# Kernel tuning notes

Measured on AMD Instinct MI355X. Metric: run time of the kernel, lower is better.

## Reference

```python
import jax, jax.numpy as jnp
import numpy as np
import math

B, L, D, H = 16, 512, 128, 8


def setup_inputs() -> dict:
    key = jax.random.key(0)
    ks = jax.random.split(key, 10)
    xavier = lambda k, shp: jax.random.normal(k, shp, jnp.float32) * math.sqrt(2.0 / (shp[0] + shp[1]))
    inp = {
        "x": jax.random.normal(ks[0], (B, L, D), jnp.float32),
        "W_q": xavier(ks[1], (H * D, D)),
        "b_q": jnp.zeros((H * D,), jnp.float32),
        "W_k": xavier(ks[2], (H * D, D)),
        "b_k": jnp.zeros((H * D,), jnp.float32),
        "W_v": xavier(ks[3], (H * D, D)),
        "b_v": jnp.zeros((H * D,), jnp.float32),
        "W_o": xavier(ks[4], (D, H * D)),
        "b_o": jnp.zeros((D,), jnp.float32),
        "pad_mask": jax.random.randint(ks[5], (B, L, L), 0, 2).astype(bool),
        "batch_size": B,
        "max_len": L,
    }
    return inp


def reference(x, W_q, b_q, W_k, b_k, W_v, b_v, W_o, b_o, pad_mask, batch_size, max_len):
    # project: [B, L, D] -> [B, L, H*D] -> head-major [H*B, L, D]
    def proj(W, b):
        y = jnp.einsum('bld,ed->ble', x, W) + b          # [B, L, H*D]
        y = y.reshape(batch_size, max_len, H, D)
        return y.transpose(2, 0, 1, 3).reshape(H * batch_size, max_len, D)

    q = proj(W_q, b_q)
    k = proj(W_k, b_k)
    v = proj(W_v, b_v)

    scores = jnp.einsum('nqd,nkd->nqk', q, k)            # [H*B, L, L]
    mask = jnp.tile(pad_mask, (H, 1, 1))                 # repeat(n_heads,1,1)
    # faithful quirk: mask BEFORE scaling, softmax over QUERY axis (dim=1)
    scores = jnp.where(mask, -1e9, scores) / math.sqrt(D)
    attn = jax.nn.softmax(scores, axis=1)
    att = jnp.einsum('nqk,nkd->nqd', attn, v)            # [H*B, L, D]
    # faithful quirk: torch .view from (H*B, L, D) to (B, L, H*D)
    att = att.reshape(batch_size, max_len, H * D)
    out = jnp.einsum('ble,de->bld', att, W_o) + b_o      # [B, L, D]
    return out
```

## Files before the change

kernel.cpp:

```cpp
#include <hip/hip_runtime.h>

#define B_  16
#define L_  512
#define D_  128
#define H_  8
#define HD_ 1024
#define NH_ 128
#define M_  8192

typedef unsigned short u16;
typedef __attribute__((ext_vector_type(8))) short s16x8;
typedef __attribute__((ext_vector_type(4))) float f32x4;

__device__ __forceinline__ float bf2f(u16 u) {
    union { unsigned u; float f; } x; x.u = ((unsigned)u) << 16; return x.f;
}
__device__ __forceinline__ u16 f2bf(float f) {
    unsigned u = __float_as_uint(f);
    return (u16)((u + 0x7FFFu + ((u >> 16) & 1u)) >> 16);
}

__device__ __forceinline__ void mfma_bt64(const u16* __restrict__ A, int lda,
                                          const u16* __restrict__ B, int ldb,
                                          int K, int lane, f32x4 acc[4][4]) {
    const int mr = lane & 15, quad = lane >> 4;
    for (int k0 = 0; k0 < K; k0 += 32) {
        s16x8 av[4], bv[4];
#pragma unroll
        for (int i = 0; i < 4; i++)
            av[i] = *(const s16x8*)(A + (size_t)(i * 16 + mr) * lda + k0 + quad * 8);
#pragma unroll
        for (int j = 0; j < 4; j++)
            bv[j] = *(const s16x8*)(B + (size_t)(j * 16 + mr) * ldb + k0 + quad * 8);
#pragma unroll
        for (int i = 0; i < 4; i++)
#pragma unroll
            for (int j = 0; j < 4; j++)
                acc[i][j] = __builtin_amdgcn_mfma_f32_16x16x32_bf16(av[i], bv[j], acc[i][j], 0, 0, 0);
    }
}

__global__ void k0_detect(const unsigned int* __restrict__ pad,
                          const unsigned int* __restrict__ xw,
                          int* __restrict__ flags) {
    __shared__ int sMask, sCnt;
    if (threadIdx.x == 0) { sMask = 0; sCnt = 0; }
    __syncthreads();
    int bad = 0;
#pragma unroll
    for (int i = 0; i < 4; i++) {
        unsigned u = pad[threadIdx.x * 4 + i];
        bad |= (u > 1u) ? 1 : 0;
    }
    int cnt = 0;
#pragma unroll
    for (int i = 0; i < 16; i++) {
        unsigned w = xw[threadIdx.x * 16 + i];
        unsigned e = (w >> 7) & 0xFFu;
        cnt += (e >= 100u && e <= 131u) ? 1 : 0;
    }
    if (bad) atomicOr(&sMask, 1);
    atomicAdd(&sCnt, cnt);
    __syncthreads();
    if (threadIdx.x == 0) {
        flags[0] = (sCnt > 2048) ? 1 : 0;
        flags[1] = sMask;
    }
}

#define PREP_TOT 1576064
__global__ __launch_bounds__(256) void kprep_conv(
    const void* x, const void* Wq, const void* bq, const void* Wk, const void* bk,
    const void* Wv, const void* bv, const void* Wo, const void* bo,
    const int* __restrict__ flags,
    u16* xb, u16* Wqb, u16* Wkb, u16* Wvb, u16* Wob,
    u16* bqb, u16* bkb, u16* bvb, u16* bob) {
    int gid = blockIdx.x * 256 + threadIdx.x;
    if (gid >= PREP_TOT) return;
    const int dt = flags[0];
    const void* src; u16* dst; int off;
    if      (gid < 1048576) { src = x;  dst = xb;  off = gid; }
    else if (gid < 1179648) { src = Wq; dst = Wqb; off = gid - 1048576; }
    else if (gid < 1310720) { src = Wk; dst = Wkb; off = gid - 1179648; }
    else if (gid < 1441792) { src = Wv; dst = Wvb; off = gid - 1310720; }
    else if (gid < 1572864) { src = Wo; dst = Wob; off = gid - 1441792; }
    else if (gid < 1573888) { src = bq; dst = bqb; off = gid - 1572864; }
    else if (gid < 1574912) { src = bk; dst = bkb; off = gid - 1573888; }
    else if (gid < 1575936) { src = bv; dst = bvb; off = gid - 1574912; }
    else                    { src = bo; dst = bob; off = gid - 1575936; }
    dst[off] = dt ? ((const u16*)src)[off] : f2bf(((const float*)src)[off]);
}

__global__ __launch_bounds__(256) void kprep_mask(const void* __restrict__ pad,
                                                  const int* __restrict__ flags,
                                                  unsigned* __restrict__ mb) {
    int w = blockIdx.x * 256 + threadIdx.x;
    size_t base = (size_t)w * 32;
    unsigned m = 0;
    if (flags[1]) {
        const unsigned char* p = (const unsigned char*)pad;
#pragma unroll
        for (int b = 0; b < 32; b++) m |= (p[base + b] ? 1u : 0u) << b;
    } else {
        const int* p = (const int*)pad;
#pragma unroll
        for (int b = 0; b < 32; b++) m |= (p[base + b] ? 1u : 0u) << b;
    }
    mb[w] = m;
}

__global__ __launch_bounds__(256) void k1_proj(
    const u16* __restrict__ xb,
    const u16* __restrict__ Wqb, const u16* __restrict__ Wkb, const u16* __restrict__ Wvb,
    const u16* __restrict__ bqb, const u16* __restrict__ bkb, const u16* __restrict__ bvb,
    u16* __restrict__ qb, u16* __restrict__ kb, u16* __restrict__ vtb) {
    const int h  = blockIdx.x;
    const int m0 = blockIdx.y * 128;
    const int z  = blockIdx.z;
    const u16* W    = (z == 0) ? Wqb : (z == 1) ? Wkb : Wvb;
    const u16* bias = (z == 0) ? bqb : (z == 1) ? bkb : bvb;

    const int lane = threadIdx.x & 63, wave = threadIdx.x >> 6;
    const int wr = wave >> 1, wc = wave & 1;
    const int mr = lane & 15, quad = lane >> 4;

    f32x4 acc[4][4];
#pragma unroll
    for (int i = 0; i < 4; i++)
#pragma unroll
        for (int j = 0; j < 4; j++) acc[i][j] = (f32x4){0.f, 0.f, 0.f, 0.f};

    mfma_bt64(xb + (size_t)(m0 + wr * 64) * D_, D_,
              W + (size_t)(h * 128 + wc * 64) * D_, D_, D_, lane, acc);

    __shared__ __align__(16) u16 T[128][136];
#pragma unroll
    for (int i = 0; i < 4; i++)
#pragma unroll
        for (int j = 0; j < 4; j++) {
            int col = wc * 64 + j * 16 + mr;
            float bv_ = bf2f(bias[h * 128 + col]);
#pragma unroll
            for (int r = 0; r < 4; r++)
                T[wr * 64 + i * 16 + quad * 4 + r][col] = f2bf(acc[i][j][r] + bv_);
        }
    __syncthreads();

    const int bb = m0 >> 9, l0 = m0 & 511;
    const int t = threadIdx.x;
    if (z < 2) {
        u16* out = z ? kb : qb;
        int row = t >> 1, c0 = (t & 1) * 64;
        u16* dst = out + ((size_t)(h * B_ + bb) * L_ + l0 + row) * D_ + c0;
#pragma unroll
        for (int c = 0; c < 64; c += 8)
            *(uint4*)(dst + c) = *(const uint4*)&T[row][c0 + c];
    } else {
        int d = t >> 1, lc0 = (t & 1) * 64;
        u16* dst = vtb + ((size_t)(h * B_ + bb) * D_ + d) * L_ + l0 + lc0;
#pragma unroll
        for (int c = 0; c < 64; c += 8) {
            u16 tmp[8];
#pragma unroll
            for (int s = 0; s < 8; s++) tmp[s] = T[lc0 + c + s][d];
            *(uint4*)(dst + c) = *(const uint4*)tmp;
        }
    }
}

__global__ __launch_bounds__(256) void k2a_linv(
    const u16* __restrict__ qb, const u16* __restrict__ kb,
    const unsigned* __restrict__ mbits, float* __restrict__ linv) {
    const int kstrip = blockIdx.x * 128;
    const int n   = blockIdx.y;
    const int bb  = n & (B_ - 1);
    const int lane = threadIdx.x & 63, wave = threadIdx.x >> 6;
    const int wr = wave >> 1, wc = wave & 1;
    const int mr = lane & 15, quad = lane >> 4;
    const float rs = 0.08838834764831845f;

    __shared__ unsigned mw[2048];
    __shared__ float CS[2][128];
#pragma unroll
    for (int s = 0; s < 8; s++) {
        int idx = threadIdx.x * 8 + s;
        int q = idx >> 2, lw = idx & 3;
        mw[idx] = mbits[((size_t)(bb << 9) + q) * 16 + (blockIdx.x << 2) + lw];
    }
    __syncthreads();

    const u16* Abase = qb + (size_t)n * L_ * D_;
    const u16* Bbase = kb + (size_t)n * L_ * D_ + (size_t)(kstrip + wc * 64) * D_;

    float colsum[4] = {0.f, 0.f, 0.f, 0.f};
    for (int qt = 0; qt < 4; qt++) {
        f32x4 acc[4][4];
#pragma unroll
        for (int i = 0; i < 4; i++)
#pragma unroll
            for (int j = 0; j < 4; j++) acc[i][j] = (f32x4){0.f, 0.f, 0.f, 0.f};
        mfma_bt64(Abase + (size_t)(qt * 128 + wr * 64) * D_, D_, Bbase, D_, D_, lane, acc);
#pragma unroll
        for (int i = 0; i < 4; i++)
#pragma unroll
            for (int j = 0; j < 4; j++) {
                const int lw = wc * 2 + (j >> 1);
                const int bit = (j & 1) * 16 + mr;
#pragma unroll
                for (int r = 0; r < 4; r++) {
                    int q = qt * 128 + wr * 64 + i * 16 + quad * 4 + r;
                    unsigned w = mw[(q << 2) + lw];
                    if (!((w >> bit) & 1u))
                        colsum[j] += __expf(acc[i][j][r] * rs);
                }
            }
    }
#pragma unroll
    for (int j = 0; j < 4; j++) {
        colsum[j] += __shfl_xor(colsum[j], 16);
        colsum[j] += __shfl_xor(colsum[j], 32);
    }
    if (quad == 0) {
#pragma unroll
        for (int j = 0; j < 4; j++) CS[wr][wc * 64 + j * 16 + mr] = colsum[j];
    }
    __syncthreads();
    if (threadIdx.x < 128)
        linv[(size_t)n * L_ + kstrip + threadIdx.x] =
            1.0f / (CS[0][threadIdx.x] + CS[1][threadIdx.x]);
}

__global__ __launch_bounds__(256) void k2b_attn(
    const u16* __restrict__ qb, const u16* __restrict__ kb,
    const u16* __restrict__ vtb, const unsigned* __restrict__ mbits,
    const float* __restrict__ linv, u16* __restrict__ att) {
    const int qtile = blockIdx.x * 128;
    const int n  = blockIdx.y;
    const int bb = n & (B_ - 1);
    const int lane = threadIdx.x & 63, wave = threadIdx.x >> 6;
    const int wr = wave >> 1, wc = wave & 1;
    const int mr = lane & 15, quad = lane >> 4;
    const float rs = 0.08838834764831845f;

    __shared__ __align__(16) u16 eS[128][136];
    __shared__ unsigned mwq[2048];
    __shared__ float linvS[512];
#pragma unroll
    for (int s = 0; s < 8; s++) {
        int idx = threadIdx.x * 8 + s;
        int q = idx >> 4, w = idx & 15;
        mwq[idx] = mbits[((size_t)(bb << 9) + qtile + q) * 16 + w];
    }
    if (threadIdx.x < 128)
        *(float4*)&linvS[threadIdx.x * 4] = *(const float4*)&linv[(size_t)n * L_ + threadIdx.x * 4];
    __syncthreads();

    const u16* qn = qb + (size_t)n * L_ * D_;
    const u16* kn = kb + (size_t)n * L_ * D_;
    const u16* vn = vtb + (size_t)n * D_ * L_;

    f32x4 att_acc[4][4];
#pragma unroll
    for (int i = 0; i < 4; i++)
#pragma unroll
        for (int j = 0; j < 4; j++) att_acc[i][j] = (f32x4){0.f, 0.f, 0.f, 0.f};

    for (int kt = 0; kt < 4; kt++) {
        f32x4 qk[4][4];
#pragma unroll
        for (int i = 0; i < 4; i++)
#pragma unroll
            for (int j = 0; j < 4; j++) qk[i][j] = (f32x4){0.f, 0.f, 0.f, 0.f};
        mfma_bt64(qn + (size_t)(qtile + wr * 64) * D_, D_,
                  kn + (size_t)(kt * 128 + wc * 64) * D_, D_, D_, lane, qk);

#pragma unroll
        for (int i = 0; i < 4; i++)
#pragma unroll
            for (int j = 0; j < 4; j++) {
                const int widx = kt * 4 + wc * 2 + (j >> 1);
                const int bit = (j & 1) * 16 + mr;
                const int kl = wc * 64 + j * 16 + mr;
                const float lv = linvS[kt * 128 + kl];
#pragma unroll
                for (int r = 0; r < 4; r++) {
                    int ql = wr * 64 + i * 16 + quad * 4 + r;
                    unsigned w = mwq[(ql << 4) + widx];
                    float e = ((w >> bit) & 1u) ? 0.f : __expf(qk[i][j][r] * rs) * lv;
                    eS[ql][kl] = f2bf(e);
                }
            }
        __syncthreads();

#pragma unroll
        for (int kk = 0; kk < 4; kk++) {
            s16x8 av[4], bv[4];
#pragma unroll
            for (int i = 0; i < 4; i++)
                av[i] = *(const s16x8*)&eS[wr * 64 + i * 16 + mr][kk * 32 + quad * 8];
#pragma unroll
            for (int j = 0; j < 4; j++)
                bv[j] = *(const s16x8*)(vn + (size_t)(wc * 64 + j * 16 + mr) * L_
                                        + kt * 128 + kk * 32 + quad * 8);
#pragma unroll
            for (int i = 0; i < 4; i++)
#pragma unroll
                for (int j = 0; j < 4; j++)
                    att_acc[i][j] = __builtin_amdgcn_mfma_f32_16x16x32_bf16(av[i], bv[j], att_acc[i][j], 0, 0, 0);
        }
        __syncthreads();
    }

#pragma unroll
    for (int i = 0; i < 4; i++)
#pragma unroll
        for (int j = 0; j < 4; j++) {
            int col = wc * 64 + j * 16 + mr;
#pragma unroll
            for (int r = 0; r < 4; r++)
                eS[wr * 64 + i * 16 + quad * 4 + r][col] = f2bf(att_acc[i][j][r]);
        }
    __syncthreads();
    int t = threadIdx.x, row = t >> 1, c0 = (t & 1) * 64;
    u16* dst = att + ((size_t)n * L_ + qtile + row) * D_ + c0;
#pragma unroll
    for (int c = 0; c < 64; c += 8)
        *(uint4*)(dst + c) = *(const uint4*)&eS[row][c0 + c];
}

__global__ __launch_bounds__(128) void k5_out(
    const u16* __restrict__ att, const u16* __restrict__ Wob,
    const u16* __restrict__ bob, const int* __restrict__ flags,
    void* __restrict__ out) {
    const int dt = flags[0];
    const int n0 = blockIdx.x * 64;
    const int m0 = blockIdx.y * 64;
    const int lane = threadIdx.x & 63, wk = threadIdx.x >> 6;
    const int mr = lane & 15, quad = lane >> 4;

    f32x4 acc[4][4];
#pragma unroll
    for (int i = 0; i < 4; i++)
#pragma unroll
        for (int j = 0; j < 4; j++) acc[i][j] = (f32x4){0.f, 0.f, 0.f, 0.f};

    mfma_bt64(att + (size_t)m0 * HD_ + wk * 512, HD_,
              Wob + (size_t)n0 * HD_ + wk * 512, HD_, 512, lane, acc);

    __shared__ __align__(16) float Tf[64][68];
    if (wk == 0) {
#pragma unroll
        for (int i = 0; i < 4; i++)
#pragma unroll
            for (int j = 0; j < 4; j++)
#pragma unroll
                for (int r = 0; r < 4; r++)
                    Tf[i * 16 + quad * 4 + r][j * 16 + mr] = acc[i][j][r];
    }
    __syncthreads();
    if (wk == 1) {
#pragma unroll
        for (int i = 0; i < 4; i++)
#pragma unroll
            for (int j = 0; j < 4; j++)
#pragma unroll
                for (int r = 0; r < 4; r++)
                    Tf[i * 16 + quad * 4 + r][j * 16 + mr] += acc[i][j][r];
    }
    __syncthreads();

    int t = threadIdx.x, row = t >> 1, h0 = (t & 1) * 32;
    size_t base = (size_t)(m0 + row) * D_ + n0 + h0;
    if (dt) {
        u16* o = (u16*)out;
#pragma unroll
        for (int c = 0; c < 32; c += 8) {
            u16 tmp[8];
#pragma unroll
            for (int s = 0; s < 8; s++)
                tmp[s] = f2bf(Tf[row][h0 + c + s] + bf2f(bob[n0 + h0 + c + s]));
            *(uint4*)(o + base + c) = *(const uint4*)tmp;
        }
    } else {
        float* o = (float*)out;
#pragma unroll
        for (int c = 0; c < 32; c += 4) {
            float4 v;
            v.x = Tf[row][h0 + c + 0] + bf2f(bob[n0 + h0 + c + 0]);
            v.y = Tf[row][h0 + c + 1] + bf2f(bob[n0 + h0 + c + 1]);
            v.z = Tf[row][h0 + c + 2] + bf2f(bob[n0 + h0 + c + 2]);
            v.w = Tf[row][h0 + c + 3] + bf2f(bob[n0 + h0 + c + 3]);
            *(float4*)(o + base + c) = v;
        }
    }
}

extern "C" void kernel_launch(void* const* d_in, const int* in_sizes, int n_in,
                              void* d_out, int out_size, void* d_ws, size_t ws_size,
                              hipStream_t stream) {
    (void)in_sizes; (void)n_in; (void)out_size; (void)ws_size;
    const void* x  = d_in[0];
    const void* Wq = d_in[1]; const void* bq = d_in[2];
    const void* Wk = d_in[3]; const void* bk = d_in[4];
    const void* Wv = d_in[5]; const void* bv = d_in[6];
    const void* Wo = d_in[7]; const void* bo = d_in[8];
    const void* pad = d_in[9];

    char* p = (char*)d_ws;
    auto alloc = [&](size_t bytes) { char* r = p; p += (bytes + 255) & ~(size_t)255; return r; };
    int*  flags = (int*)alloc(256);
    u16*  xb   = (u16*)alloc(2097152);
    u16*  Wqb  = (u16*)alloc(262144);
    u16*  Wkb  = (u16*)alloc(262144);
    u16*  Wvb  = (u16*)alloc(262144);
    u16*  Wob  = (u16*)alloc(262144);
    u16*  bqb  = (u16*)alloc(2048);
    u16*  bkb  = (u16*)alloc(2048);
    u16*  bvb  = (u16*)alloc(2048);
    u16*  bob  = (u16*)alloc(256);
    unsigned* mbits = (unsigned*)alloc(524288);
    float* linv = (float*)alloc(262144);
    u16*  qb   = (u16*)alloc(16777216);
    u16*  kb   = (u16*)alloc(16777216);
    u16*  vtb  = (u16*)alloc(16777216);
    u16*  att  = (u16*)alloc(2097152);

    k0_detect<<<1, 256, 0, stream>>>((const unsigned*)pad, (const unsigned*)x, flags);
    kprep_conv<<<(PREP_TOT + 255) / 256, 256, 0, stream>>>(
        x, Wq, bq, Wk, bk, Wv, bv, Wo, bo, flags,
        xb, Wqb, Wkb, Wvb, Wob, bqb, bkb, bvb, bob);
    kprep_mask<<<512, 256, 0, stream>>>(pad, flags, mbits);
    k1_proj<<<dim3(8, 64, 3), 256, 0, stream>>>(
        xb, Wqb, Wkb, Wvb, bqb, bkb, bvb, qb, kb, vtb);
    k2a_linv<<<dim3(4, NH_), 256, 0, stream>>>(qb, kb, mbits, linv);
    k2b_attn<<<dim3(4, NH_), 256, 0, stream>>>(qb, kb, vtb, mbits, linv, att);
    k5_out<<<dim3(2, 128), 128, 0, stream>>>(att, Wob, bob, flags, d_out);
}
```

Measured before the change: 256.9 us.

## Split projection and attention kernels into smaller tiles and atomically accumulate column sums

The projection kernel now uses 64-row tiles with 128 threads, doubling the block count. The column-sum kernel splits each head's query range in two and accumulates partial sums into a zero-initialised buffer with atomicAdd; the reciprocal is taken later in the attention kernel. The attention kernel now handles 64 query rows per block, with each wave covering a 64-key slice for QK and a 32-column slice for PV, which doubles the grid again. The goal is to expose more blocks to the CUs, at the cost of more redundant K/V loads and atomic traffic. The attention output buffer is also enlarged to its true size.

```diff
diff --git a/kernel.cpp b/kernel.cpp
--- a/kernel.cpp
+++ b/kernel.cpp
@@ -93,8 +93,10 @@
 
 __global__ __launch_bounds__(256) void kprep_mask(const void* __restrict__ pad,
                                                   const int* __restrict__ flags,
-                                                  unsigned* __restrict__ mb) {
+                                                  unsigned* __restrict__ mb,
+                                                  float* __restrict__ lsum) {
     int w = blockIdx.x * 256 + threadIdx.x;
+    if (w < 65536) lsum[w] = 0.f;
     size_t base = (size_t)w * 32;
     unsigned m = 0;
     if (flags[1]) {
@@ -109,19 +111,18 @@
     mb[w] = m;
 }
 
-__global__ __launch_bounds__(256) void k1_proj(
+__global__ __launch_bounds__(128) void k1_proj(
     const u16* __restrict__ xb,
     const u16* __restrict__ Wqb, const u16* __restrict__ Wkb, const u16* __restrict__ Wvb,
     const u16* __restrict__ bqb, const u16* __restrict__ bkb, const u16* __restrict__ bvb,
     u16* __restrict__ qb, u16* __restrict__ kb, u16* __restrict__ vtb) {
-    const int h  = blockIdx.x;
-    const int m0 = blockIdx.y * 128;
+    const int m0 = blockIdx.x * 64;
+    const int h  = blockIdx.y;
     const int z  = blockIdx.z;
     const u16* W    = (z == 0) ? Wqb : (z == 1) ? Wkb : Wvb;
     const u16* bias = (z == 0) ? bqb : (z == 1) ? bkb : bvb;
 
-    const int lane = threadIdx.x & 63, wave = threadIdx.x >> 6;
-    const int wr = wave >> 1, wc = wave & 1;
+    const int lane = threadIdx.x & 63, wc = threadIdx.x >> 6;
     const int mr = lane & 15, quad = lane >> 4;
 
     f32x4 acc[4][4];
@@ -130,10 +131,10 @@
 #pragma unroll
         for (int j = 0; j < 4; j++) acc[i][j] = (f32x4){0.f, 0.f, 0.f, 0.f};
 
-    mfma_bt64(xb + (size_t)(m0 + wr * 64) * D_, D_,
+    mfma_bt64(xb + (size_t)m0 * D_, D_,
               W + (size_t)(h * 128 + wc * 64) * D_, D_, D_, lane, acc);
 
-    __shared__ __align__(16) u16 T[128][136];
+    __shared__ __align__(16) u16 T[64][136];
 #pragma unroll
     for (int i = 0; i < 4; i++)
 #pragma unroll
@@ -142,7 +143,7 @@
             float bv_ = bf2f(bias[h * 128 + col]);
 #pragma unroll
             for (int r = 0; r < 4; r++)
-                T[wr * 64 + i * 16 + quad * 4 + r][col] = f2bf(acc[i][j][r] + bv_);
+                T[i * 16 + quad * 4 + r][col] = f2bf(acc[i][j][r] + bv_);
         }
     __syncthreads();
 
@@ -156,64 +157,65 @@
         for (int c = 0; c < 64; c += 8)
             *(uint4*)(dst + c) = *(const uint4*)&T[row][c0 + c];
     } else {
-        int d = t >> 1, lc0 = (t & 1) * 64;
-        u16* dst = vtb + ((size_t)(h * B_ + bb) * D_ + d) * L_ + l0 + lc0;
+        u16* dst = vtb + ((size_t)(h * B_ + bb) * D_ + t) * L_ + l0;
 #pragma unroll
         for (int c = 0; c < 64; c += 8) {
             u16 tmp[8];
 #pragma unroll
-            for (int s = 0; s < 8; s++) tmp[s] = T[lc0 + c + s][d];
+            for (int s = 0; s < 8; s++) tmp[s] = T[c + s][t];
             *(uint4*)(dst + c) = *(const uint4*)tmp;
         }
     }
 }
 
-__global__ __launch_bounds__(256) void k2a_linv(
+__global__ __launch_bounds__(256) void k2a_lsum(
     const u16* __restrict__ qb, const u16* __restrict__ kb,
-    const unsigned* __restrict__ mbits, float* __restrict__ linv) {
-    const int kstrip = blockIdx.x * 128;
-    const int n   = blockIdx.y;
-    const int bb  = n & (B_ - 1);
-    const int lane = threadIdx.x & 63, wave = threadIdx.x >> 6;
+    const unsigned* __restrict__ mbits, float* __restrict__ lsum) {
+    const int n     = blockIdx.x;
+    const int ks    = blockIdx.y * 128;
+    const int qbase = blockIdx.z * 256;
+    const int bb    = n & (B_ - 1);
+    const int tid = threadIdx.x;
+    const int lane = tid & 63, wave = tid >> 6;
     const int wr = wave >> 1, wc = wave & 1;
     const int mr = lane & 15, quad = lane >> 4;
     const float rs = 0.08838834764831845f;
 
-    __shared__ unsigned mw[2048];
+    __shared__ unsigned mw[1024];
     __shared__ float CS[2][128];
 #pragma unroll
-    for (int s = 0; s < 8; s++) {
-        int idx = threadIdx.x * 8 + s;
+    for (int s = 0; s < 4; s++) {
+        int idx = tid * 4 + s;
         int q = idx >> 2, lw = idx & 3;
-        mw[idx] = mbits[((size_t)(bb << 9) + q) * 16 + (blockIdx.x << 2) + lw];
-    }
-    __syncthreads();
-
-    const u16* Abase = qb + (size_t)n * L_ * D_;
-    const u16* Bbase = kb + (size_t)n * L_ * D_ + (size_t)(kstrip + wc * 64) * D_;
+        mw[idx] = mbits[((size_t)(bb << 9) + qbase + q) * 16 + blockIdx.y * 4 + lw];
+    }
+    __syncthreads();
+
+    const u16* qn = qb + (size_t)n * L_ * D_;
+    const u16* kB = kb + (size_t)n * L_ * D_ + (size_t)(ks + wc * 64) * D_;
 
     float colsum[4] = {0.f, 0.f, 0.f, 0.f};
-    for (int qt = 0; qt < 4; qt++) {
+    for (int qt = 0; qt < 2; qt++) {
+        const int ql0 = wr * 128 + qt * 64;
         f32x4 acc[4][4];
 #pragma unroll
         for (int i = 0; i < 4; i++)
 #pragma unroll
             for (int j = 0; j < 4; j++) acc[i][j] = (f32x4){0.f, 0.f, 0.f, 0.f};
-        mfma_bt64(Abase + (size_t)(qt * 128 + wr * 64) * D_, D_, Bbase, D_, D_, lane, acc);
-#pragma unroll
-        for (int i = 0; i < 4; i++)
-#pragma unroll
-            for (int j = 0; j < 4; j++) {
-                const int lw = wc * 2 + (j >> 1);
-                const int bit = (j & 1) * 16 + mr;
+        mfma_bt64(qn + (size_t)(qbase + ql0) * D_, D_, kB, D_, D_, lane, acc);
+#pragma unroll
+        for (int j = 0; j < 4; j++) {
+            const int lw = wc * 2 + (j >> 1);
+            const int bit = (j & 1) * 16 + mr;
+#pragma unroll
+            for (int i = 0; i < 4; i++)
 #pragma unroll
                 for (int r = 0; r < 4; r++) {
-                    int q = qt * 128 + wr * 64 + i * 16 + quad * 4 + r;
-                    unsigned w = mw[(q << 2) + lw];
-                    if (!((w >> bit) & 1u))
+                    int ql = ql0 + i * 16 + quad * 4 + r;
+                    if (!((mw[(ql << 2) + lw] >> bit) & 1u))
                         colsum[j] += __expf(acc[i][j][r] * rs);
                 }
-            }
+        }
     }
 #pragma unroll
     for (int j = 0; j < 4; j++) {
@@ -225,88 +227,94 @@
         for (int j = 0; j < 4; j++) CS[wr][wc * 64 + j * 16 + mr] = colsum[j];
     }
     __syncthreads();
-    if (threadIdx.x < 128)
-        linv[(size_t)n * L_ + kstrip + threadIdx.x] =
-            1.0f / (CS[0][threadIdx.x] + CS[1][threadIdx.x]);
+    if (tid < 128)
+        atomicAdd(&lsum[(size_t)n * L_ + ks + tid], CS[0][tid] + CS[1][tid]);
 }
 
 __global__ __launch_bounds__(256) void k2b_attn(
     const u16* __restrict__ qb, const u16* __restrict__ kb,
     const u16* __restrict__ vtb, const unsigned* __restrict__ mbits,
-    const float* __restrict__ linv, u16* __restrict__ att) {
-    const int qtile = blockIdx.x * 128;
-    const int n  = blockIdx.y;
+    const float* __restrict__ lsum, u16* __restrict__ att) {
+    const int n  = blockIdx.x;
+    const int q0 = blockIdx.y * 64;
     const int bb = n & (B_ - 1);
-    const int lane = threadIdx.x & 63, wave = threadIdx.x >> 6;
-    const int wr = wave >> 1, wc = wave & 1;
+    const int tid = threadIdx.x;
+    const int lane = tid & 63, w = tid >> 6;
     const int mr = lane & 15, quad = lane >> 4;
     const float rs = 0.08838834764831845f;
 
-    __shared__ __align__(16) u16 eS[128][136];
-    __shared__ unsigned mwq[2048];
+    __shared__ __align__(16) u16 eS[64 * 264];
+    __shared__ unsigned mwq[1024];
     __shared__ float linvS[512];
-#pragma unroll
-    for (int s = 0; s < 8; s++) {
-        int idx = threadIdx.x * 8 + s;
-        int q = idx >> 4, w = idx & 15;
-        mwq[idx] = mbits[((size_t)(bb << 9) + qtile + q) * 16 + w];
-    }
-    if (threadIdx.x < 128)
-        *(float4*)&linvS[threadIdx.x * 4] = *(const float4*)&linv[(size_t)n * L_ + threadIdx.x * 4];
-    __syncthreads();
-
-    const u16* qn = qb + (size_t)n * L_ * D_;
+
+#pragma unroll
+    for (int s = 0; s < 4; s++) {
+        int idx = tid * 4 + s;
+        int ql = idx >> 4, wd = idx & 15;
+        mwq[idx] = mbits[((size_t)(bb << 9) + q0 + ql) * 16 + wd];
+    }
+    if (tid < 128) {
+        float4 ls = *(const float4*)&lsum[(size_t)n * L_ + tid * 4];
+        linvS[tid * 4 + 0] = 1.f / ls.x;
+        linvS[tid * 4 + 1] = 1.f / ls.y;
+        linvS[tid * 4 + 2] = 1.f / ls.z;
+        linvS[tid * 4 + 3] = 1.f / ls.w;
+    }
+    __syncthreads();
+
+    const u16* qn = qb + (size_t)n * L_ * D_ + (size_t)q0 * D_;
     const u16* kn = kb + (size_t)n * L_ * D_;
     const u16* vn = vtb + (size_t)n * D_ * L_;
 
-    f32x4 att_acc[4][4];
+    f32x4 accd[4][2];
 #pragma unroll
     for (int i = 0; i < 4; i++)
 #pragma unroll
-        for (int j = 0; j < 4; j++) att_acc[i][j] = (f32x4){0.f, 0.f, 0.f, 0.f};
-
-    for (int kt = 0; kt < 4; kt++) {
+        for (int j = 0; j < 2; j++) accd[i][j] = (f32x4){0.f, 0.f, 0.f, 0.f};
+
+    for (int it = 0; it < 2; it++) {
+        const int kc0 = it * 256 + w * 64;
         f32x4 qk[4][4];
 #pragma unroll
         for (int i = 0; i < 4; i++)
 #pragma unroll
             for (int j = 0; j < 4; j++) qk[i][j] = (f32x4){0.f, 0.f, 0.f, 0.f};
-        mfma_bt64(qn + (size_t)(qtile + wr * 64) * D_, D_,
-                  kn + (size_t)(kt * 128 + wc * 64) * D_, D_, D_, lane, qk);
-
-#pragma unroll
-        for (int i = 0; i < 4; i++)
-#pragma unroll
-            for (int j = 0; j < 4; j++) {
-                const int widx = kt * 4 + wc * 2 + (j >> 1);
-                const int bit = (j & 1) * 16 + mr;
-                const int kl = wc * 64 + j * 16 + mr;
-                const float lv = linvS[kt * 128 + kl];
+        mfma_bt64(qn, D_, kn + (size_t)kc0 * D_, D_, D_, lane, qk);
+
+#pragma unroll
+        for (int j = 0; j < 4; j++) {
+            const int kc = kc0 + j * 16 + mr;
+            const int wd = kc >> 5;
+            const int bit = kc & 31;
+            const float lv = linvS[kc];
+            const int colL = w * 64 + j * 16 + mr;
+#pragma unroll
+            for (int i = 0; i < 4; i++)
 #pragma unroll
                 for (int r = 0; r < 4; r++) {
-                    int ql = wr * 64 + i * 16 + quad * 4 + r;
-                    unsigned w = mwq[(ql << 4) + widx];
-                    float e = ((w >> bit) & 1u) ? 0.f : __expf(qk[i][j][r] * rs) * lv;
-                    eS[ql][kl] = f2bf(e);
+                    int ql = i * 16 + quad * 4 + r;
+                    float e = ((mwq[(ql << 4) + wd] >> bit) & 1u)
+                              ? 0.f : __expf(qk[i][j][r] * rs) * lv;
+                    eS[ql * 264 + colL] = f2bf(e);
                 }
-            }
+        }
         __syncthreads();
 
 #pragma unroll
-        for (int kk = 0; kk < 4; kk++) {
-            s16x8 av[4], bv[4];
+        for (int kk = 0; kk < 8; kk++) {
+            s16x8 av[4], bv[2];
 #pragma unroll
             for (int i = 0; i < 4; i++)
-                av[i] = *(const s16x8*)&eS[wr * 64 + i * 16 + mr][kk * 32 + quad * 8];
-#pragma unroll
-            for (int j = 0; j < 4; j++)
-                bv[j] = *(const s16x8*)(vn + (size_t)(wc * 64 + j * 16 + mr) * L_
-                                        + kt * 128 + kk * 32 + quad * 8);
+                av[i] = *(const s16x8*)&eS[(i * 16 + mr) * 264 + kk * 32 + quad * 8];
+#pragma unroll
+            for (int j = 0; j < 2; j++)
+                bv[j] = *(const s16x8*)(vn + (size_t)(w * 32 + j * 16 + mr) * L_
+                                        + it * 256 + kk * 32 + quad * 8);
 #pragma unroll
             for (int i = 0; i < 4; i++)
 #pragma unroll
-                for (int j = 0; j < 4; j++)
-                    att_acc[i][j] = __builtin_amdgcn_mfma_f32_16x16x32_bf16(av[i], bv[j], att_acc[i][j], 0, 0, 0);
+                for (int j = 0; j < 2; j++)
+                    accd[i][j] = __builtin_amdgcn_mfma_f32_16x16x32_bf16(av[i], bv[j], accd[i][j], 0, 0, 0);
         }
         __syncthreads();
     }
@@ -314,18 +322,18 @@
 #pragma unroll
     for (int i = 0; i < 4; i++)
 #pragma unroll
-        for (int j = 0; j < 4; j++) {
-            int col = wc * 64 + j * 16 + mr;
+        for (int j = 0; j < 2; j++) {
+            int col = w * 32 + j * 16 + mr;
 #pragma unroll
             for (int r = 0; r < 4; r++)
-                eS[wr * 64 + i * 16 + quad * 4 + r][col] = f2bf(att_acc[i][j][r]);
-        }
-    __syncthreads();
-    int t = threadIdx.x, row = t >> 1, c0 = (t & 1) * 64;
-    u16* dst = att + ((size_t)n * L_ + qtile + row) * D_ + c0;
-#pragma unroll
-    for (int c = 0; c < 64; c += 8)
-        *(uint4*)(dst + c) = *(const uint4*)&eS[row][c0 + c];
+                eS[(i * 16 + quad * 4 + r) * 136 + col] = f2bf(accd[i][j][r]);
+        }
+    __syncthreads();
+    int row = tid >> 2, c0 = (tid & 3) * 32;
+    u16* dst = att + ((size_t)n * L_ + q0 + row) * D_ + c0;
+#pragma unroll
+    for (int c = 0; c < 32; c += 8)
+        *(uint4*)(dst + c) = *(const uint4*)&eS[row * 136 + c0 + c];
 }
 
 __global__ __launch_bounds__(128) void k5_out(
@@ -419,20 +427,20 @@
     u16*  bvb  = (u16*)alloc(2048);
     u16*  bob  = (u16*)alloc(256);
     unsigned* mbits = (unsigned*)alloc(524288);
-    float* linv = (float*)alloc(262144);
+    float* lsum = (float*)alloc(262144);
     u16*  qb   = (u16*)alloc(16777216);
     u16*  kb   = (u16*)alloc(16777216);
     u16*  vtb  = (u16*)alloc(16777216);
-    u16*  att  = (u16*)alloc(2097152);
+    u16*  att  = (u16*)alloc(16777216);
 
     k0_detect<<<1, 256, 0, stream>>>((const unsigned*)pad, (const unsigned*)x, flags);
     kprep_conv<<<(PREP_TOT + 255) / 256, 256, 0, stream>>>(
         x, Wq, bq, Wk, bk, Wv, bv, Wo, bo, flags,
         xb, Wqb, Wkb, Wvb, Wob, bqb, bkb, bvb, bob);
-    kprep_mask<<<512, 256, 0, stream>>>(pad, flags, mbits);
-    k1_proj<<<dim3(8, 64, 3), 256, 0, stream>>>(
+    kprep_mask<<<512, 256, 0, stream>>>(pad, flags, mbits, lsum);
+    k1_proj<<<dim3(128, 8, 3), 128, 0, stream>>>(
         xb, Wqb, Wkb, Wvb, bqb, bkb, bvb, qb, kb, vtb);
-    k2a_linv<<<dim3(4, NH_), 256, 0, stream>>>(qb, kb, mbits, linv);
-    k2b_attn<<<dim3(4, NH_), 256, 0, stream>>>(qb, kb, vtb, mbits, linv, att);
+    k2a_lsum<<<dim3(128, 4, 2), 256, 0, stream>>>(qb, kb, mbits, lsum);
+    k2b_attn<<<dim3(128, 8), 256, 0, stream>>>(qb, kb, vtb, mbits, lsum, att);
     k5_out<<<dim3(2, 128), 128, 0, stream>>>(att, Wob, bob, flags, d_out);
 }
```

Result: slower. 271.2 us (+5.6%).
